# Performance work log

Hardware: AMD Instinct MI355X
Metric: run time of the kernel (lower is better)

The kernel has to match this reference:

```python
import jax, jax.numpy as jnp
import numpy as np

LOG2PI = 1.8378770664093453  # log(2*pi)
TEMP = 0.5  # Gumbel-softmax resampling temperature


def setup_inputs() -> dict:
    key = jax.random.key(0)
    ks = jax.random.split(key, 32)
    B, N, T = 16, 512, 16
    dL, dM, dE, H = 128, 256, 32, 256
    Kt, Ka = 18, 8  # k_regimes + 10 total slots, 8 active
    dIn = dM + dL + dE  # proposal input dim = 416
    r = jax.random.normal

    def w(k, shape):
        return r(k, shape, dtype=jnp.float32) / np.sqrt(shape[0]).astype(np.float32)

    return {
        "obs": r(ks[0], (T, B), dtype=jnp.float32),
        "h_seq": r(ks[1], (T, B, dM), dtype=jnp.float32),
        "z0": r(ks[2], (B, N, dL), dtype=jnp.float32),
        "regime_logits0": r(ks[3], (B, N, Kt), dtype=jnp.float32),
        "eps": r(ks[4], (T, B, N, dL), dtype=jnp.float32),
        "gumbel_u": jax.random.uniform(ks[5], (T, B, N, N), dtype=jnp.float32),
        # LearnedProposal params
        "pe_emb": w(ks[6], (Kt, dE)),
        "pz_w1": w(ks[7], (dIn, H)), "pz_b1": jnp.zeros((H,)),
        "pz_w2": w(ks[8], (H, H)), "pz_b2": jnp.zeros((H,)),
        "pz_w3": w(ks[9], (H, 2 * dL)), "pz_b3": jnp.zeros((2 * dL,)),
        "pr_w1": w(ks[10], (dIn, H)), "pr_b1": jnp.zeros((H,)),
        "pr_w2": w(ks[11], (H, 8)), "pr_b2": jnp.zeros((8,)),
        # ObservationV3 params
        "oe_w1": w(ks[12], (dL + dM, 256)), "oe_b1": jnp.zeros((256,)),
        "oe_w2": w(ks[13], (256, 128)), "oe_b2": jnp.zeros((128,)),
        "oe_w3": w(ks[14], (128, 2)), "oe_b3": jnp.zeros((2,)),
        "log_obs_scale": jnp.zeros((Kt,)),
        "k_active": 8,
    }


def reference(obs, h_seq, z0, regime_logits0, eps, gumbel_u,
              pe_emb, pz_w1, pz_b1, pz_w2, pz_b2, pz_w3, pz_b3,
              pr_w1, pr_b1, pr_w2, pr_b2,
              oe_w1, oe_b1, oe_w2, oe_b2, oe_w3, oe_b3,
              log_obs_scale, k_active):
    B, N, dL = z0.shape
    Kt = regime_logits0.shape[-1]
    silu = jax.nn.silu
    emb_a = pe_emb[:k_active]                               # (Ka, dE)
    scales = jax.nn.softplus(log_obs_scale[:k_active])      # (Ka,)

    def step(carry, xs):
        z, rl, log_w = carry
        h_t, y_t, eps_t, u_t = xs
        h_exp = jnp.broadcast_to(h_t[:, None, :], (B, N, h_t.shape[-1]))
        # --- LearnedProposal ---
        rp = jax.nn.softmax(rl, axis=-1)[:, :, :k_active]
        remb = rp @ emb_a                                   # (B,N,dE)
        inp = jnp.concatenate([h_exp, z, remb], axis=-1)
        hz = silu(inp @ pz_w1 + pz_b1)
        hz = silu(hz @ pz_w2 + pz_b2)
        zp = hz @ pz_w3 + pz_b3
        z_mean = zp[..., :dL]
        z_log_std = jnp.clip(zp[..., dL:], -5.0, 2.0)
        z_new = z_mean + eps_t * jnp.exp(z_log_std)
        log_q = jnp.sum(-0.5 * eps_t**2 - z_log_std - 0.5 * LOG2PI, axis=-1)
        rlog = silu(inp @ pr_w1 + pr_b1) @ pr_w2 + pr_b2    # (B,N,Ka)
        rlog = jnp.concatenate(
            [rlog, jnp.zeros((B, N, Kt - rlog.shape[-1]), rlog.dtype)], axis=-1)
        # --- ObservationV3.log_likelihood ---
        em = silu(jnp.concatenate([z_new, h_exp], axis=-1) @ oe_w1 + oe_b1)
        em = silu(em @ oe_w2 + oe_b2)
        em = em @ oe_w3 + oe_b3
        pred, lsb = em[..., 0], em[..., 1]
        rp_new = jax.nn.softmax(rlog, axis=-1)[:, :, :k_active]
        sigma = jnp.clip(jax.nn.softplus(lsb) * (rp_new @ scales), 0.1, 5.0)
        ll = -0.5 * ((y_t[:, None] - pred) / sigma)**2 - jnp.log(sigma) - 0.5 * LOG2PI
        log_w = log_w + ll - log_q
        # weighted mean output (before resampling resets weights)
        w = jax.nn.softmax(log_w, axis=-1)
        mean_z = jnp.sum(w[..., None] * z_new, axis=1)      # (B,dL)
        # --- soft_resample_v3 (Gumbel-softmax bmm) ---
        g = -jnp.log(-jnp.log(u_t + 1e-10) + 1e-10)
        A = jax.nn.softmax((log_w[:, None, :] + g) / TEMP, axis=-1)  # (B,N,N)
        z_r = jnp.einsum('bij,bjd->bid', A, z_new)
        rl_r = jnp.einsum('bij,bjk->bik', A, rlog)
        return (z_r, rl_r, jnp.zeros_like(log_w)), mean_z

    init = (z0, regime_logits0, jnp.zeros((B, N), z0.dtype))
    _, means = jax.lax.scan(step, init, (h_seq, obs, eps, gumbel_u))
    return means  # (T, B, d_latent)
```

## Files before the change

kernel.cpp:

```cpp
#include <hip/hip_runtime.h>
#include <hip/hip_bf16.h>
#include <math.h>

#define LOG2PI 1.8378770664093453f

constexpr int Bb = 16, Nn = 512, Tt = 16;
constexpr int dL = 128, dM = 256, dE = 32, Kt = 18;
constexpr int P = Bb * Nn;
constexpr int BLK = 32;
constexpr int LDA = 520;
constexpr int LDB = 264;
constexpr int LDE = 136;
constexpr int LDZX = 132;
constexpr int LDR = 40;

typedef __attribute__((ext_vector_type(8))) _Float16 f16x8;
typedef __attribute__((ext_vector_type(4))) float f32x4;

__device__ __forceinline__ float siluf(float x) { return x / (1.f + expf(-x)); }
__device__ __forceinline__ float softplusf(float x) {
    return (x > 20.f) ? x : log1pf(expf(x));
}
__device__ __forceinline__ short f2h(float x) {
    _Float16 h = (_Float16)x;
    short s;
    __builtin_memcpy(&s, &h, 2);
    return s;
}
__device__ __forceinline__ float h2f(short s) {
    _Float16 h;
    __builtin_memcpy(&h, &s, 2);
    return (float)h;
}
__device__ __forceinline__ void split2(float x, short& hi, short& lo) {
    hi = f2h(x);
    lo = f2h(x - h2f(hi));
}
__device__ __forceinline__ f32x4 mfma16(f16x8 a, f16x8 b, f32x4 c) {
    return __builtin_amdgcn_mfma_f32_16x16x32_f16(a, b, c, 0, 0, 0);
}

template<int NF>
__device__ __forceinline__ void mfma_bn(
    const f16x8 (&ah)[2], const f16x8 (&al)[2],
    const short* __restrict__ Whi, const short* __restrict__ Wlo,
    int Kw, int k0, int n0, int lr, int lk, f32x4 (&acc)[2][NF])
{
    #pragma unroll
    for (int nf = 0; nf < NF; nf++) {
        size_t bo = (size_t)(n0 + nf * 16 + lr) * Kw + k0 + lk;
        f16x8 bh = *reinterpret_cast<const f16x8*>(Whi + bo);
        f16x8 bl = *reinterpret_cast<const f16x8*>(Wlo + bo);
        #pragma unroll
        for (int mf = 0; mf < 2; mf++) {
            acc[mf][nf] = mfma16(ah[mf], bh, acc[mf][nf]);
            acc[mf][nf] = mfma16(ah[mf], bl, acc[mf][nf]);
            acc[mf][nf] = mfma16(al[mf], bh, acc[mf][nf]);
        }
    }
}

template<int NF, int KB, int KE, int KW>
__device__ __forceinline__ void gemm_lds(
    const short* lAhi, const short* lAlo, int ldA, int akoff,
    const short* __restrict__ Whi, const short* __restrict__ Wlo,
    int n0, int lr, int lk, f32x4 (&acc)[2][NF])
{
    #pragma unroll 2
    for (int k0 = KB; k0 < KE; k0 += 32) {
        f16x8 ah[2], al[2];
        #pragma unroll
        for (int mf = 0; mf < 2; mf++) {
            int ao = (mf * 16 + lr) * ldA + (k0 - akoff) + lk;
            ah[mf] = *reinterpret_cast<const f16x8*>(lAhi + ao);
            al[mf] = *reinterpret_cast<const f16x8*>(lAlo + ao);
        }
        mfma_bn<NF>(ah, al, Whi, Wlo, KW, k0, n0, lr, lk, acc);
    }
}

template<int NF>
__device__ __forceinline__ void epi_silu(
    f32x4 (&acc)[2][NF], const float* biasw,
    short* outHi, short* outLo, int ldOut, int outBase, int lr, int l4)
{
    #pragma unroll
    for (int nf = 0; nf < NF; nf++) {
        float bv = biasw[nf * 16 + lr];
        #pragma unroll
        for (int mf = 0; mf < 2; mf++) {
            #pragma unroll
            for (int r = 0; r < 4; r++) {
                int row = mf * 16 + l4 + r;
                int col = outBase + nf * 16 + lr;
                float sv = siluf(acc[mf][nf][r] + bv);
                short hi, lo;
                split2(sv, hi, lo);
                outHi[row * ldOut + col] = hi;
                outLo[row * ldOut + col] = lo;
            }
        }
    }
}

struct SMem {
    short actAhi[BLK * LDA], actAlo[BLK * LDA];
    short actBhi[BLK * LDB], actBlo[BLK * LDB];
    short e2hi[BLK * LDE], e2lo[BLK * LDE];
    short hhhi[256], hhlo[256];
    short rembhi[BLK * LDR], remblo[BLK * LDR];
    float zlsx[BLK * LDZX];
    float peL[256];
    float probs[BLK * 8];
    float rlogL[BLK * 8];
    float lqp[4 * BLK];
};

__global__ __launch_bounds__(512) void mega(
    const float* __restrict__ zc, const float* __restrict__ rl,
    const float* __restrict__ h_t, const float* __restrict__ pe_emb,
    const float* __restrict__ eps_t, const float* __restrict__ obs_t,
    const short* __restrict__ w_l1h, const short* __restrict__ w_l1l,
    const short* __restrict__ w_pz2h, const short* __restrict__ w_pz2l,
    const short* __restrict__ w_pz3h, const short* __restrict__ w_pz3l,
    const short* __restrict__ w_oe1h, const short* __restrict__ w_oe1l,
    const short* __restrict__ w_oe2h, const short* __restrict__ w_oe2l,
    const float* __restrict__ pz_b1, const float* __restrict__ pr_b1,
    const float* __restrict__ pz_b2, const float* __restrict__ pz_b3,
    const float* __restrict__ oe_b1, const float* __restrict__ oe_b2,
    const float* __restrict__ pr_w2, const float* __restrict__ pr_b2,
    const float* __restrict__ oe_w3, const float* __restrict__ oe_b3,
    const float* __restrict__ los,
    float* __restrict__ log_w,
    short* __restrict__ vthi, short* __restrict__ vtlo)
{
    __shared__ SMem sm;
    const int tid = threadIdx.x;
    const int wv = tid >> 6, l = tid & 63;
    const int lr = l & 15, lk = (l >> 4) * 8, l4 = (l >> 4) * 4;
    const int p0 = blockIdx.x * BLK;
    const int b = p0 >> 9;
    const int i0 = p0 & 511;

    {
        if (tid < 256) {
            const float* hb = h_t + b * dM;
            short hi, lo;
            split2(hb[tid], hi, lo);
            sm.hhhi[tid] = hi; sm.hhlo[tid] = lo;
            sm.peL[tid] = pe_emb[tid];
        } else {
            int q = tid - 256;
            int pp = q >> 3, cc = q & 7;
            vthi[((size_t)b * 144 + 136 + cc) * 512 + i0 + pp] = 0;
            vtlo[((size_t)b * 144 + 136 + cc) * 512 + i0 + pp] = 0;
        }
        if (tid < BLK) {
            int p = tid;
            float v[Kt], m = -1e30f;
            #pragma unroll
            for (int k = 0; k < Kt; k++) {
                v[k] = rl[(size_t)(p0 + p) * Kt + k];
                m = fmaxf(m, v[k]);
            }
            float denom = 0.f;
            #pragma unroll
            for (int k = 0; k < Kt; k++) denom += expf(v[k] - m);
            #pragma unroll
            for (int k = 0; k < 8; k++)
                sm.probs[p * 8 + k] = expf(v[k] - m) / denom;
        }
    }
    __syncthreads();
    {
        #pragma unroll
        for (int it = 0; it < 2; it++) {
            int idx = it * 512 + tid;
            int p = idx >> 5, d = idx & 31;
            float acc = 0.f;
            #pragma unroll
            for (int kk = 0; kk < 8; kk++)
                acc = fmaf(sm.probs[p * 8 + kk], sm.peL[kk * 32 + d], acc);
            short hi, lo;
            split2(acc, hi, lo);
            sm.rembhi[p * LDR + d] = hi;
            sm.remblo[p * LDR + d] = lo;
        }
    }
    __syncthreads();

    {
        f32x4 acc1[2][4];
        #pragma unroll
        for (int mf = 0; mf < 2; mf++)
            #pragma unroll
            for (int nf = 0; nf < 4; nf++) acc1[mf][nf] = f32x4{0.f, 0.f, 0.f, 0.f};
        int n0 = wv * 64;
        gemm_lds<4, 0, 256, 416>(sm.hhhi, sm.hhlo, 0, 0, w_l1h, w_l1l, n0, lr, lk, acc1);
        #pragma unroll 2
        for (int k0 = 256; k0 < 384; k0 += 32) {
            f16x8 ah[2], al[2];
            #pragma unroll
            for (int mf = 0; mf < 2; mf++) {
                const float* zr = zc + (size_t)(p0 + mf * 16 + lr) * dL + (k0 - 256) + lk;
                #pragma unroll
                for (int j = 0; j < 8; j++) {
                    float zv = zr[j];
                    _Float16 h = (_Float16)zv;
                    ah[mf][j] = h;
                    al[mf][j] = (_Float16)(zv - (float)h);
                }
            }
            mfma_bn<4>(ah, al, w_l1h, w_l1l, 416, k0, n0, lr, lk, acc1);
        }
        gemm_lds<4, 384, 416, 416>(sm.rembhi, sm.remblo, LDR, 384, w_l1h, w_l1l, n0, lr, lk, acc1);
        const float* biasw = (n0 < 256) ? (pz_b1 + n0) : (pr_b1 + (n0 - 256));
        epi_silu<4>(acc1, biasw, sm.actAhi, sm.actAlo, LDA, n0, lr, l4);
    }
    __syncthreads();

    {
        f32x4 acc2[2][2];
        #pragma unroll
        for (int mf = 0; mf < 2; mf++)
            #pragma unroll
            for (int nf = 0; nf < 2; nf++) acc2[mf][nf] = f32x4{0.f, 0.f, 0.f, 0.f};
        int n0 = wv * 32;
        gemm_lds<2, 0, 256, 256>(sm.actAhi, sm.actAlo, LDA, 0, w_pz2h, w_pz2l, n0, lr, lk, acc2);
        epi_silu<2>(acc2, pz_b2 + n0, sm.actBhi, sm.actBlo, LDB, n0, lr, l4);
    }
    __syncthreads();

    {
        f32x4 acc3[2][2];
        #pragma unroll
        for (int mf = 0; mf < 2; mf++)
            #pragma unroll
            for (int nf = 0; nf < 2; nf++) acc3[mf][nf] = f32x4{0.f, 0.f, 0.f, 0.f};
        int n0 = wv * 32;
        gemm_lds<2, 0, 256, 256>(sm.actBhi, sm.actBlo, LDB, 0, w_pz3h, w_pz3l, n0, lr, lk, acc3);
        if (wv >= 4) {
            #pragma unroll
            for (int nf = 0; nf < 2; nf++) {
                int col = n0 + nf * 16 + lr;
                float bv = pz_b3[col];
                #pragma unroll
                for (int mf = 0; mf < 2; mf++)
                    #pragma unroll
                    for (int r = 0; r < 4; r++) {
                        int row = mf * 16 + l4 + r;
                        float zls = fminf(fmaxf(acc3[mf][nf][r] + bv, -5.f), 2.f);
                        sm.zlsx[row * LDZX + (col - 128)] = zls;
                    }
            }
        }
        __syncthreads();
        if (wv < 4) {
            float rowsum[8] = {};
            #pragma unroll
            for (int nf = 0; nf < 2; nf++) {
                int d = n0 + nf * 16 + lr;
                float bv = pz_b3[d];
                #pragma unroll
                for (int mf = 0; mf < 2; mf++)
                    #pragma unroll
                    for (int r = 0; r < 4; r++) {
                        int row = mf * 16 + l4 + r;
                        float zm = acc3[mf][nf][r] + bv;
                        float zls = sm.zlsx[row * LDZX + d];
                        float e = eps_t[(size_t)(p0 + row) * dL + d];
                        float zn = zm + e * expf(zls);
                        short hi, lo;
                        split2(zn, hi, lo);
                        sm.e2hi[row * LDE + d] = hi;
                        sm.e2lo[row * LDE + d] = lo;
                        rowsum[mf * 4 + r] += -0.5f * e * e - zls;
                    }
            }
            #pragma unroll
            for (int o = 1; o < 16; o <<= 1)
                #pragma unroll
                for (int j = 0; j < 8; j++)
                    rowsum[j] += __shfl_xor(rowsum[j], o);
            if (lr == 0) {
                #pragma unroll
                for (int j = 0; j < 8; j++) {
                    int row = (j >> 2) * 16 + l4 + (j & 3);
                    sm.lqp[wv * BLK + row] = rowsum[j];
                }
            }
        }
    }
    __syncthreads();

    #pragma unroll
    for (int it = 0; it < 8; it++) {
        int idx = it * 512 + tid;
        int d = idx >> 5, row = idx & 31;
        vthi[((size_t)b * 144 + d) * 512 + i0 + row] = sm.e2hi[row * LDE + d];
        vtlo[((size_t)b * 144 + d) * 512 + i0 + row] = sm.e2lo[row * LDE + d];
    }

    {
        int p = tid >> 4, s = tid & 15;
        float a8[8] = {};
        for (int kk = s * 16; kk < s * 16 + 16; kk++) {
            float hv = h2f(sm.actAhi[p * LDA + 256 + kk]) +
                       h2f(sm.actAlo[p * LDA + 256 + kk]);
            #pragma unroll
            for (int r = 0; r < 8; r++) a8[r] = fmaf(hv, pr_w2[kk * 8 + r], a8[r]);
        }
        #pragma unroll
        for (int o = 1; o < 16; o <<= 1)
            #pragma unroll
            for (int r = 0; r < 8; r++) a8[r] += __shfl_xor(a8[r], o);
        if (s == 0) {
            #pragma unroll
            for (int r = 0; r < 8; r++) {
                float v = a8[r] + pr_b2[r];
                sm.rlogL[p * 8 + r] = v;
                short hi, lo;
                split2(v, hi, lo);
                vthi[((size_t)b * 144 + 128 + r) * 512 + i0 + p] = hi;
                vtlo[((size_t)b * 144 + 128 + r) * 512 + i0 + p] = lo;
            }
        }
    }
    __syncthreads();

    {
        f32x4 acc5[2][2];
        #pragma unroll
        for (int mf = 0; mf < 2; mf++)
            #pragma unroll
            for (int nf = 0; nf < 2; nf++) acc5[mf][nf] = f32x4{0.f, 0.f, 0.f, 0.f};
        int n0 = wv * 32;
        gemm_lds<2, 0, 256, 384>(sm.hhhi, sm.hhlo, 0, 0, w_oe1h, w_oe1l, n0, lr, lk, acc5);
        gemm_lds<2, 256, 384, 384>(sm.e2hi, sm.e2lo, LDE, 256, w_oe1h, w_oe1l, n0, lr, lk, acc5);
        __syncthreads();
        epi_silu<2>(acc5, oe_b1 + n0, sm.actAhi, sm.actAlo, LDA, n0, lr, l4);
    }
    __syncthreads();

    {
        f32x4 acc6[2][1];
        #pragma unroll
        for (int mf = 0; mf < 2; mf++) acc6[mf][0] = f32x4{0.f, 0.f, 0.f, 0.f};
        int n0 = wv * 16;
        gemm_lds<1, 0, 256, 256>(sm.actAhi, sm.actAlo, LDA, 0, w_oe2h, w_oe2l, n0, lr, lk, acc6);
        __syncthreads();
        epi_silu<1>(acc6, oe_b2 + n0, sm.e2hi, sm.e2lo, LDE, n0, lr, l4);
    }
    __syncthreads();

    {
        int p = tid >> 4, s = tid & 15;
        float q0 = 0.f, q1 = 0.f;
        for (int k = s * 8; k < s * 8 + 8; k++) {
            float e = h2f(sm.e2hi[p * LDE + k]) + h2f(sm.e2lo[p * LDE + k]);
            q0 = fmaf(e, oe_w3[2 * k], q0);
            q1 = fmaf(e, oe_w3[2 * k + 1], q1);
        }
        #pragma unroll
        for (int o = 1; o < 16; o <<= 1) {
            q0 += __shfl_xor(q0, o);
            q1 += __shfl_xor(q1, o);
        }
        if (s == 0) {
            float pred = q0 + oe_b3[0];
            float lsb  = q1 + oe_b3[1];
            float rv[8], m = 0.f;
            #pragma unroll
            for (int r = 0; r < 8; r++) {
                rv[r] = sm.rlogL[p * 8 + r];
                m = fmaxf(m, rv[r]);
            }
            float denom = (Kt - 8) * expf(-m);
            #pragma unroll
            for (int r = 0; r < 8; r++) denom += expf(rv[r] - m);
            float sdot = 0.f;
            #pragma unroll
            for (int r = 0; r < 8; r++)
                sdot += (expf(rv[r] - m) / denom) * softplusf(los[r]);
            float sigma = fminf(fmaxf(softplusf(lsb) * sdot, 0.1f), 5.f);
            float y = obs_t[b];
            float dd = (y - pred) / sigma;
            float ll = -0.5f * dd * dd - logf(sigma) - 0.5f * LOG2PI;
            float lq = sm.lqp[p] + sm.lqp[BLK + p] + sm.lqp[2 * BLK + p]
                     + sm.lqp[3 * BLK + p] - dL * 0.5f * LOG2PI;
            log_w[p0 + p] = ll - lq;
        }
    }
}

__global__ __launch_bounds__(256) void kT(
    const float* __restrict__ in, short* __restrict__ oh, short* __restrict__ ol,
    int K, int N, int ostride, int ooff)
{
    int idx = blockIdx.x * 256 + threadIdx.x;
    if (idx < K * N) {
        int n = idx / K, k = idx % K;
        short hi, lo;
        split2(in[(size_t)k * N + n], hi, lo);
        oh[(size_t)n * ostride + ooff + k] = hi;
        ol[(size_t)n * ostride + ooff + k] = lo;
    }
}

__global__ __launch_bounds__(256) void k11x(
    const float* __restrict__ log_w, const float* __restrict__ u_t,
    short* __restrict__ Ahi, short* __restrict__ Alo,
    short* __restrict__ Ameanhi, short* __restrict__ Ameanlo,
    float* __restrict__ rl)
{
    int wave = threadIdx.x >> 6, lane = threadIdx.x & 63;
    if (blockIdx.x < P / 4) {
        int row = blockIdx.x * 4 + wave;
        int b = row >> 9;
        float q[8], m = -1e30f;
        #pragma unroll
        for (int jj = 0; jj < 8; jj++) {
            int j = jj * 64 + lane;
            float u = u_t[(size_t)row * Nn + j];
            float g = -logf(-logf(u + 1e-10f) + 1e-10f);
            q[jj] = (log_w[b * Nn + j] + g) * 2.0f;
            m = fmaxf(m, q[jj]);
        }
        #pragma unroll
        for (int o = 1; o < 64; o <<= 1) m = fmaxf(m, __shfl_xor(m, o));
        float e[8], s = 0.f;
        #pragma unroll
        for (int jj = 0; jj < 8; jj++) { e[jj] = expf(q[jj] - m); s += e[jj]; }
        #pragma unroll
        for (int o = 1; o < 64; o <<= 1) s += __shfl_xor(s, o);
        float inv = 1.f / s;
        #pragma unroll
        for (int jj = 0; jj < 8; jj++) {
            short hi, lo;
            split2(e[jj] * inv, hi, lo);
            Ahi[(size_t)row * Nn + jj * 64 + lane] = hi;
            Alo[(size_t)row * Nn + jj * 64 + lane] = lo;
        }
        if (lane < 10) rl[row * Kt + 8 + lane] = 0.f;
    } else {
        int b = (blockIdx.x - P / 4) * 4 + wave;
        float q[8], m = -1e30f;
        #pragma unroll
        for (int jj = 0; jj < 8; jj++) {
            q[jj] = log_w[b * Nn + jj * 64 + lane];
            m = fmaxf(m, q[jj]);
        }
        #pragma unroll
        for (int o = 1; o < 64; o <<= 1) m = fmaxf(m, __shfl_xor(m, o));
        float e[8], s = 0.f;
        #pragma unroll
        for (int jj = 0; jj < 8; jj++) { e[jj] = expf(q[jj] - m); s += e[jj]; }
        #pragma unroll
        for (int o = 1; o < 64; o <<= 1) s += __shfl_xor(s, o);
        float inv = 1.f / s;
        #pragma unroll
        for (int jj = 0; jj < 8; jj++) {
            short hi, lo;
            split2(e[jj] * inv, hi, lo);
            Ameanhi[(size_t)b * Nn + jj * 64 + lane] = hi;
            Ameanlo[(size_t)b * Nn + jj * 64 + lane] = lo;
        }
    }
}

__global__ __launch_bounds__(256) void k12x(
    const short* __restrict__ Ahi, const short* __restrict__ Alo,
    const short* __restrict__ Ameanhi, const short* __restrict__ Ameanlo,
    const short* __restrict__ vthi, const short* __restrict__ vtlo,
    float* __restrict__ z, float* __restrict__ rl, float* __restrict__ out_t)
{
    int tid = threadIdx.x;
    int w = tid >> 6, l = tid & 63;
    int lr = l & 15, lk = (l >> 4) * 8;
    int b = blockIdx.x;
    int n0 = blockIdx.z * 48;
    size_t voff = ((size_t)b * 144 + n0 + lr) * 512 + lk;

    if (blockIdx.y == 8) {
        if (w != 0) return;
        f32x4 acc[3];
        #pragma unroll
        for (int nf = 0; nf < 3; nf++) acc[nf] = f32x4{0.f, 0.f, 0.f, 0.f};
        for (int k0 = 0; k0 < 512; k0 += 32) {
            f16x8 ah, al;
            #pragma unroll
            for (int j = 0; j < 8; j++) { ah[j] = (_Float16)0.f; al[j] = (_Float16)0.f; }
            if (lr == 0) {
                ah = *reinterpret_cast<const f16x8*>(Ameanhi + (size_t)b * Nn + k0 + lk);
                al = *reinterpret_cast<const f16x8*>(Ameanlo + (size_t)b * Nn + k0 + lk);
            }
            #pragma unroll
            for (int nf = 0; nf < 3; nf++) {
                size_t bo = voff + (size_t)nf * 16 * 512 + k0;
                f16x8 bh = *reinterpret_cast<const f16x8*>(vthi + bo);
                f16x8 bl = *reinterpret_cast<const f16x8*>(vtlo + bo);
                acc[nf] = mfma16(ah, bh, acc[nf]);
                acc[nf] = mfma16(ah, bl, acc[nf]);
                acc[nf] = mfma16(al, bh, acc[nf]);
            }
        }
        if ((l >> 4) == 0) {
            #pragma unroll
            for (int nf = 0; nf < 3; nf++) {
                int col = n0 + nf * 16 + lr;
                if (col < 128) out_t[b * dL + col] = acc[nf][0];
            }
        }
        return;
    }

    int m0 = blockIdx.y * 64 + w * 16;
    size_t aoff = ((size_t)(b * 512 + m0 + lr)) * 512 + lk;
    f32x4 acc[3];
    #pragma unroll
    for (int nf = 0; nf < 3; nf++) acc[nf] = f32x4{0.f, 0.f, 0.f, 0.f};
    for (int k0 = 0; k0 < 512; k0 += 32) {
        f16x8 ah = *reinterpret_cast<const f16x8*>(Ahi + aoff + k0);
        f16x8 al = *reinterpret_cast<const f16x8*>(Alo + aoff + k0);
        #pragma unroll
        for (int nf = 0; nf < 3; nf++) {
            size_t bo = voff + (size_t)nf * 16 * 512 + k0;
            f16x8 bh = *reinterpret_cast<const f16x8*>(vthi + bo);
            f16x8 bl = *reinterpret_cast<const f16x8*>(vtlo + bo);
            acc[nf] = mfma16(ah, bh, acc[nf]);
            acc[nf] = mfma16(ah, bl, acc[nf]);
            acc[nf] = mfma16(al, bh, acc[nf]);
        }
    }
    int orow = (l >> 4) * 4;
    #pragma unroll
    for (int nf = 0; nf < 3; nf++) {
        int col = n0 + nf * 16 + lr;
        #pragma unroll
        for (int r = 0; r < 4; r++) {
            int gp = b * 512 + m0 + orow + r;
            float v = acc[nf][r];
            if (col < 128) z[(size_t)gp * dL + col] = v;
            else if (col < 136) rl[gp * Kt + (col - 128)] = v;
        }
    }
}

extern "C" void kernel_launch(void* const* d_in, const int* in_sizes, int n_in,
                              void* d_out, int out_size, void* d_ws, size_t ws_size,
                              hipStream_t stream)
{
    const float* obs      = (const float*)d_in[0];
    const float* h_seq    = (const float*)d_in[1];
    const float* z0       = (const float*)d_in[2];
    const float* rl0      = (const float*)d_in[3];
    const float* eps      = (const float*)d_in[4];
    const float* gum      = (const float*)d_in[5];
    const float* pe_emb   = (const float*)d_in[6];
    const float* pz_w1    = (const float*)d_in[7];
    const float* pz_b1    = (const float*)d_in[8];
    const float* pz_w2    = (const float*)d_in[9];
    const float* pz_b2    = (const float*)d_in[10];
    const float* pz_w3    = (const float*)d_in[11];
    const float* pz_b3    = (const float*)d_in[12];
    const float* pr_w1    = (const float*)d_in[13];
    const float* pr_b1    = (const float*)d_in[14];
    const float* pr_w2    = (const float*)d_in[15];
    const float* pr_b2    = (const float*)d_in[16];
    const float* oe_w1    = (const float*)d_in[17];
    const float* oe_b1    = (const float*)d_in[18];
    const float* oe_w2    = (const float*)d_in[19];
    const float* oe_b2    = (const float*)d_in[20];
    const float* oe_w3    = (const float*)d_in[21];
    const float* oe_b3    = (const float*)d_in[22];
    const float* los      = (const float*)d_in[23];
    float* out = (float*)d_out;

    char* base = (char*)d_ws;
    float* z      = (float*)base;  base += (size_t)P * dL * 4;
    float* rl     = (float*)base;  base += (size_t)P * Kt * 4;
    float* log_w  = (float*)base;  base += (size_t)P * 4;
    short* vthi   = (short*)base;  base += (size_t)16 * 144 * 512 * 2;
    short* vtlo   = (short*)base;  base += (size_t)16 * 144 * 512 * 2;
    short* Ahi    = (short*)base;  base += (size_t)P * 512 * 2;
    short* Alo    = (short*)base;  base += (size_t)P * 512 * 2;
    short* Amhi   = (short*)base;  base += (size_t)16 * 512 * 2;
    short* Amlo   = (short*)base;  base += (size_t)16 * 512 * 2;
    short* w_l1h  = (short*)base;  base += (size_t)512 * 416 * 2;
    short* w_l1l  = (short*)base;  base += (size_t)512 * 416 * 2;
    short* w_pz2h = (short*)base;  base += (size_t)256 * 256 * 2;
    short* w_pz2l = (short*)base;  base += (size_t)256 * 256 * 2;
    short* w_pz3h = (short*)base;  base += (size_t)256 * 256 * 2;
    short* w_pz3l = (short*)base;  base += (size_t)256 * 256 * 2;
    short* w_oe1h = (short*)base;  base += (size_t)256 * 384 * 2;
    short* w_oe1l = (short*)base;  base += (size_t)256 * 384 * 2;
    short* w_oe2h = (short*)base;  base += (size_t)128 * 256 * 2;
    short* w_oe2l = (short*)base;  base += (size_t)128 * 256 * 2;

    kT<<<(416 * 256 + 255) / 256, 256, 0, stream>>>(pz_w1, w_l1h, w_l1l, 416, 256, 416, 0);
    kT<<<(416 * 256 + 255) / 256, 256, 0, stream>>>(
        pr_w1, w_l1h + (size_t)256 * 416, w_l1l + (size_t)256 * 416, 416, 256, 416, 0);
    kT<<<(256 * 256 + 255) / 256, 256, 0, stream>>>(pz_w2, w_pz2h, w_pz2l, 256, 256, 256, 0);
    kT<<<(256 * 256 + 255) / 256, 256, 0, stream>>>(pz_w3, w_pz3h, w_pz3l, 256, 256, 256, 0);
    kT<<<(256 * 256 + 255) / 256, 256, 0, stream>>>(
        oe_w1 + (size_t)128 * 256, w_oe1h, w_oe1l, 256, 256, 384, 0);
    kT<<<(128 * 256 + 255) / 256, 256, 0, stream>>>(
        oe_w1, w_oe1h, w_oe1l, 128, 256, 384, 256);
    kT<<<(256 * 128 + 255) / 256, 256, 0, stream>>>(oe_w2, w_oe2h, w_oe2l, 256, 128, 256, 0);

    (void)hipMemcpyAsync(z, z0, (size_t)P * dL * sizeof(float),
                         hipMemcpyDeviceToDevice, stream);
    (void)hipMemcpyAsync(rl, rl0, (size_t)P * Kt * sizeof(float),
                         hipMemcpyDeviceToDevice, stream);

    for (int t = 0; t < Tt; t++) {
        const float* h_t   = h_seq + (size_t)t * Bb * dM;
        const float* obs_t = obs + (size_t)t * Bb;
        const float* eps_t = eps + (size_t)t * P * dL;
        const float* u_t   = gum + (size_t)t * P * Nn;
        float* out_t = out + (size_t)t * Bb * dL;

        mega<<<P / BLK, 512, 0, stream>>>(
            z, rl, h_t, pe_emb, eps_t, obs_t,
            w_l1h, w_l1l, w_pz2h, w_pz2l, w_pz3h, w_pz3l,
            w_oe1h, w_oe1l, w_oe2h, w_oe2l,
            pz_b1, pr_b1, pz_b2, pz_b3, oe_b1, oe_b2,
            pr_w2, pr_b2, oe_w3, oe_b3, los,
            log_w, vthi, vtlo);
        k11x<<<P / 4 + 4, 256, 0, stream>>>(log_w, u_t, Ahi, Alo,
                                            Amhi, Amlo, rl);
        k12x<<<dim3(16, 9, 3), 256, 0, stream>>>(Ahi, Alo, Amhi, Amlo,
                                                 vthi, vtlo, z, rl, out_t);
    }
}
```

Baseline: 2.050 ms.

## Halve particle block size to 16 rows per workgroup in fused step kernel

Cuts the per-workgroup particle tile from 32 to 16 rows. The MFMA helpers, epilogues and reductions are reworked for a single 16-row fragment, and the thread-to-row mappings in the small reductions are adjusted. This doubles the number of workgroups (512 instead of 256) so the MI355X's many CUs get more work, but every weight fragment loaded from global or L2 now feeds half as many MFMAs, lowering weight reuse and arithmetic intensity.

```diff
diff --git a/kernel.cpp b/kernel.cpp
--- a/kernel.cpp
+++ b/kernel.cpp
@@ -7,7 +7,7 @@
 constexpr int Bb = 16, Nn = 512, Tt = 16;
 constexpr int dL = 128, dM = 256, dE = 32, Kt = 18;
 constexpr int P = Bb * Nn;
-constexpr int BLK = 32;
+constexpr int BLK = 16;
 constexpr int LDA = 520;
 constexpr int LDB = 264;
 constexpr int LDE = 136;
@@ -41,64 +41,54 @@
 }
 
 template<int NF>
-__device__ __forceinline__ void mfma_bn(
-    const f16x8 (&ah)[2], const f16x8 (&al)[2],
+__device__ __forceinline__ void mfma_bn1(
+    f16x8 ah, f16x8 al,
     const short* __restrict__ Whi, const short* __restrict__ Wlo,
-    int Kw, int k0, int n0, int lr, int lk, f32x4 (&acc)[2][NF])
+    int Kw, int k0, int n0, int lr, int lk, f32x4 (&acc)[NF])
 {
     #pragma unroll
     for (int nf = 0; nf < NF; nf++) {
         size_t bo = (size_t)(n0 + nf * 16 + lr) * Kw + k0 + lk;
         f16x8 bh = *reinterpret_cast<const f16x8*>(Whi + bo);
         f16x8 bl = *reinterpret_cast<const f16x8*>(Wlo + bo);
-        #pragma unroll
-        for (int mf = 0; mf < 2; mf++) {
-            acc[mf][nf] = mfma16(ah[mf], bh, acc[mf][nf]);
-            acc[mf][nf] = mfma16(ah[mf], bl, acc[mf][nf]);
-            acc[mf][nf] = mfma16(al[mf], bh, acc[mf][nf]);
-        }
+        acc[nf] = mfma16(ah, bh, acc[nf]);
+        acc[nf] = mfma16(ah, bl, acc[nf]);
+        acc[nf] = mfma16(al, bh, acc[nf]);
     }
 }
 
 template<int NF, int KB, int KE, int KW>
-__device__ __forceinline__ void gemm_lds(
+__device__ __forceinline__ void gemm_lds1(
     const short* lAhi, const short* lAlo, int ldA, int akoff,
     const short* __restrict__ Whi, const short* __restrict__ Wlo,
-    int n0, int lr, int lk, f32x4 (&acc)[2][NF])
+    int n0, int lr, int lk, f32x4 (&acc)[NF])
 {
     #pragma unroll 2
     for (int k0 = KB; k0 < KE; k0 += 32) {
-        f16x8 ah[2], al[2];
-        #pragma unroll
-        for (int mf = 0; mf < 2; mf++) {
-            int ao = (mf * 16 + lr) * ldA + (k0 - akoff) + lk;
-            ah[mf] = *reinterpret_cast<const f16x8*>(lAhi + ao);
-            al[mf] = *reinterpret_cast<const f16x8*>(lAlo + ao);
-        }
-        mfma_bn<NF>(ah, al, Whi, Wlo, KW, k0, n0, lr, lk, acc);
+        int ao = lr * ldA + (k0 - akoff) + lk;
+        f16x8 ah = *reinterpret_cast<const f16x8*>(lAhi + ao);
+        f16x8 al = *reinterpret_cast<const f16x8*>(lAlo + ao);
+        mfma_bn1<NF>(ah, al, Whi, Wlo, KW, k0, n0, lr, lk, acc);
     }
 }
 
 template<int NF>
-__device__ __forceinline__ void epi_silu(
-    f32x4 (&acc)[2][NF], const float* biasw,
+__device__ __forceinline__ void epi_silu1(
+    f32x4 (&acc)[NF], const float* biasw,
     short* outHi, short* outLo, int ldOut, int outBase, int lr, int l4)
 {
     #pragma unroll
     for (int nf = 0; nf < NF; nf++) {
         float bv = biasw[nf * 16 + lr];
         #pragma unroll
-        for (int mf = 0; mf < 2; mf++) {
-            #pragma unroll
-            for (int r = 0; r < 4; r++) {
-                int row = mf * 16 + l4 + r;
-                int col = outBase + nf * 16 + lr;
-                float sv = siluf(acc[mf][nf][r] + bv);
-                short hi, lo;
-                split2(sv, hi, lo);
-                outHi[row * ldOut + col] = hi;
-                outLo[row * ldOut + col] = lo;
-            }
+        for (int r = 0; r < 4; r++) {
+            int row = l4 + r;
+            int col = outBase + nf * 16 + lr;
+            float sv = siluf(acc[nf][r] + bv);
+            short hi, lo;
+            split2(sv, hi, lo);
+            outHi[row * ldOut + col] = hi;
+            outLo[row * ldOut + col] = lo;
         }
     }
 }
@@ -149,7 +139,7 @@
             split2(hb[tid], hi, lo);
             sm.hhhi[tid] = hi; sm.hhlo[tid] = lo;
             sm.peL[tid] = pe_emb[tid];
-        } else {
+        } else if (tid < 384) {
             int q = tid - 256;
             int pp = q >> 3, cc = q & 7;
             vthi[((size_t)b * 144 + 136 + cc) * 512 + i0 + pp] = 0;
@@ -173,145 +163,126 @@
     }
     __syncthreads();
     {
-        #pragma unroll
-        for (int it = 0; it < 2; it++) {
-            int idx = it * 512 + tid;
-            int p = idx >> 5, d = idx & 31;
-            float acc = 0.f;
-            #pragma unroll
-            for (int kk = 0; kk < 8; kk++)
-                acc = fmaf(sm.probs[p * 8 + kk], sm.peL[kk * 32 + d], acc);
-            short hi, lo;
-            split2(acc, hi, lo);
-            sm.rembhi[p * LDR + d] = hi;
-            sm.remblo[p * LDR + d] = lo;
-        }
-    }
-    __syncthreads();
-
-    {
-        f32x4 acc1[2][4];
-        #pragma unroll
-        for (int mf = 0; mf < 2; mf++)
-            #pragma unroll
-            for (int nf = 0; nf < 4; nf++) acc1[mf][nf] = f32x4{0.f, 0.f, 0.f, 0.f};
+        int p = tid >> 5, d = tid & 31;
+        float acc = 0.f;
+        #pragma unroll
+        for (int kk = 0; kk < 8; kk++)
+            acc = fmaf(sm.probs[p * 8 + kk], sm.peL[kk * 32 + d], acc);
+        short hi, lo;
+        split2(acc, hi, lo);
+        sm.rembhi[p * LDR + d] = hi;
+        sm.remblo[p * LDR + d] = lo;
+    }
+    __syncthreads();
+
+    {
+        f32x4 acc1[4];
+        #pragma unroll
+        for (int nf = 0; nf < 4; nf++) acc1[nf] = f32x4{0.f, 0.f, 0.f, 0.f};
         int n0 = wv * 64;
-        gemm_lds<4, 0, 256, 416>(sm.hhhi, sm.hhlo, 0, 0, w_l1h, w_l1l, n0, lr, lk, acc1);
+        gemm_lds1<4, 0, 256, 416>(sm.hhhi, sm.hhlo, 0, 0, w_l1h, w_l1l, n0, lr, lk, acc1);
         #pragma unroll 2
         for (int k0 = 256; k0 < 384; k0 += 32) {
-            f16x8 ah[2], al[2];
-            #pragma unroll
-            for (int mf = 0; mf < 2; mf++) {
-                const float* zr = zc + (size_t)(p0 + mf * 16 + lr) * dL + (k0 - 256) + lk;
-                #pragma unroll
-                for (int j = 0; j < 8; j++) {
-                    float zv = zr[j];
-                    _Float16 h = (_Float16)zv;
-                    ah[mf][j] = h;
-                    al[mf][j] = (_Float16)(zv - (float)h);
-                }
-            }
-            mfma_bn<4>(ah, al, w_l1h, w_l1l, 416, k0, n0, lr, lk, acc1);
-        }
-        gemm_lds<4, 384, 416, 416>(sm.rembhi, sm.remblo, LDR, 384, w_l1h, w_l1l, n0, lr, lk, acc1);
+            f16x8 ah, al;
+            const float* zr = zc + (size_t)(p0 + lr) * dL + (k0 - 256) + lk;
+            #pragma unroll
+            for (int j = 0; j < 8; j++) {
+                float zv = zr[j];
+                _Float16 h = (_Float16)zv;
+                ah[j] = h;
+                al[j] = (_Float16)(zv - (float)h);
+            }
+            mfma_bn1<4>(ah, al, w_l1h, w_l1l, 416, k0, n0, lr, lk, acc1);
+        }
+        gemm_lds1<4, 384, 416, 416>(sm.rembhi, sm.remblo, LDR, 384, w_l1h, w_l1l, n0, lr, lk, acc1);
         const float* biasw = (n0 < 256) ? (pz_b1 + n0) : (pr_b1 + (n0 - 256));
-        epi_silu<4>(acc1, biasw, sm.actAhi, sm.actAlo, LDA, n0, lr, l4);
-    }
-    __syncthreads();
-
-    {
-        f32x4 acc2[2][2];
-        #pragma unroll
-        for (int mf = 0; mf < 2; mf++)
-            #pragma unroll
-            for (int nf = 0; nf < 2; nf++) acc2[mf][nf] = f32x4{0.f, 0.f, 0.f, 0.f};
+        epi_silu1<4>(acc1, biasw, sm.actAhi, sm.actAlo, LDA, n0, lr, l4);
+    }
+    __syncthreads();
+
+    {
+        f32x4 acc2[2];
+        acc2[0] = f32x4{0.f, 0.f, 0.f, 0.f};
+        acc2[1] = f32x4{0.f, 0.f, 0.f, 0.f};
         int n0 = wv * 32;
-        gemm_lds<2, 0, 256, 256>(sm.actAhi, sm.actAlo, LDA, 0, w_pz2h, w_pz2l, n0, lr, lk, acc2);
-        epi_silu<2>(acc2, pz_b2 + n0, sm.actBhi, sm.actBlo, LDB, n0, lr, l4);
-    }
-    __syncthreads();
-
-    {
-        f32x4 acc3[2][2];
-        #pragma unroll
-        for (int mf = 0; mf < 2; mf++)
-            #pragma unroll
-            for (int nf = 0; nf < 2; nf++) acc3[mf][nf] = f32x4{0.f, 0.f, 0.f, 0.f};
+        gemm_lds1<2, 0, 256, 256>(sm.actAhi, sm.actAlo, LDA, 0, w_pz2h, w_pz2l, n0, lr, lk, acc2);
+        epi_silu1<2>(acc2, pz_b2 + n0, sm.actBhi, sm.actBlo, LDB, n0, lr, l4);
+    }
+    __syncthreads();
+
+    {
+        f32x4 acc3[2];
+        acc3[0] = f32x4{0.f, 0.f, 0.f, 0.f};
+        acc3[1] = f32x4{0.f, 0.f, 0.f, 0.f};
         int n0 = wv * 32;
-        gemm_lds<2, 0, 256, 256>(sm.actBhi, sm.actBlo, LDB, 0, w_pz3h, w_pz3l, n0, lr, lk, acc3);
+        gemm_lds1<2, 0, 256, 256>(sm.actBhi, sm.actBlo, LDB, 0, w_pz3h, w_pz3l, n0, lr, lk, acc3);
         if (wv >= 4) {
             #pragma unroll
             for (int nf = 0; nf < 2; nf++) {
                 int col = n0 + nf * 16 + lr;
                 float bv = pz_b3[col];
                 #pragma unroll
-                for (int mf = 0; mf < 2; mf++)
-                    #pragma unroll
-                    for (int r = 0; r < 4; r++) {
-                        int row = mf * 16 + l4 + r;
-                        float zls = fminf(fmaxf(acc3[mf][nf][r] + bv, -5.f), 2.f);
-                        sm.zlsx[row * LDZX + (col - 128)] = zls;
-                    }
+                for (int r = 0; r < 4; r++) {
+                    int row = l4 + r;
+                    float zls = fminf(fmaxf(acc3[nf][r] + bv, -5.f), 2.f);
+                    sm.zlsx[row * LDZX + (col - 128)] = zls;
+                }
             }
         }
         __syncthreads();
         if (wv < 4) {
-            float rowsum[8] = {};
+            float rowsum[4] = {};
             #pragma unroll
             for (int nf = 0; nf < 2; nf++) {
                 int d = n0 + nf * 16 + lr;
                 float bv = pz_b3[d];
                 #pragma unroll
-                for (int mf = 0; mf < 2; mf++)
-                    #pragma unroll
-                    for (int r = 0; r < 4; r++) {
-                        int row = mf * 16 + l4 + r;
-                        float zm = acc3[mf][nf][r] + bv;
-                        float zls = sm.zlsx[row * LDZX + d];
-                        float e = eps_t[(size_t)(p0 + row) * dL + d];
-                        float zn = zm + e * expf(zls);
-                        short hi, lo;
-                        split2(zn, hi, lo);
-                        sm.e2hi[row * LDE + d] = hi;
-                        sm.e2lo[row * LDE + d] = lo;
-                        rowsum[mf * 4 + r] += -0.5f * e * e - zls;
-                    }
+                for (int r = 0; r < 4; r++) {
+                    int row = l4 + r;
+                    float zm = acc3[nf][r] + bv;
+                    float zls = sm.zlsx[row * LDZX + d];
+                    float e = eps_t[(size_t)(p0 + row) * dL + d];
+                    float zn = zm + e * expf(zls);
+                    short hi, lo;
+                    split2(zn, hi, lo);
+                    sm.e2hi[row * LDE + d] = hi;
+                    sm.e2lo[row * LDE + d] = lo;
+                    rowsum[r] += -0.5f * e * e - zls;
+                }
             }
             #pragma unroll
             for (int o = 1; o < 16; o <<= 1)
                 #pragma unroll
-                for (int j = 0; j < 8; j++)
+                for (int j = 0; j < 4; j++)
                     rowsum[j] += __shfl_xor(rowsum[j], o);
             if (lr == 0) {
                 #pragma unroll
-                for (int j = 0; j < 8; j++) {
-                    int row = (j >> 2) * 16 + l4 + (j & 3);
-                    sm.lqp[wv * BLK + row] = rowsum[j];
-                }
+                for (int j = 0; j < 4; j++)
+                    sm.lqp[wv * BLK + l4 + j] = rowsum[j];
             }
         }
     }
     __syncthreads();
 
     #pragma unroll
-    for (int it = 0; it < 8; it++) {
+    for (int it = 0; it < 4; it++) {
         int idx = it * 512 + tid;
-        int d = idx >> 5, row = idx & 31;
+        int d = idx >> 4, row = idx & 15;
         vthi[((size_t)b * 144 + d) * 512 + i0 + row] = sm.e2hi[row * LDE + d];
         vtlo[((size_t)b * 144 + d) * 512 + i0 + row] = sm.e2lo[row * LDE + d];
     }
 
     {
-        int p = tid >> 4, s = tid & 15;
+        int p = tid >> 5, s = tid & 31;
         float a8[8] = {};
-        for (int kk = s * 16; kk < s * 16 + 16; kk++) {
+        for (int kk = s * 8; kk < s * 8 + 8; kk++) {
             float hv = h2f(sm.actAhi[p * LDA + 256 + kk]) +
                        h2f(sm.actAlo[p * LDA + 256 + kk]);
             #pragma unroll
             for (int r = 0; r < 8; r++) a8[r] = fmaf(hv, pr_w2[kk * 8 + r], a8[r]);
         }
         #pragma unroll
-        for (int o = 1; o < 16; o <<= 1)
+        for (int o = 1; o < 32; o <<= 1)
             #pragma unroll
             for (int r = 0; r < 8; r++) a8[r] += __shfl_xor(a8[r], o);
         if (s == 0) {
@@ -329,40 +300,37 @@
     __syncthreads();
 
     {
-        f32x4 acc5[2][2];
-        #pragma unroll
-        for (int mf = 0; mf < 2; mf++)
-            #pragma unroll
-            for (int nf = 0; nf < 2; nf++) acc5[mf][nf] = f32x4{0.f, 0.f, 0.f, 0.f};
+        f32x4 acc5[2];
+        acc5[0] = f32x4{0.f, 0.f, 0.f, 0.f};
+        acc5[1] = f32x4{0.f, 0.f, 0.f, 0.f};
         int n0 = wv * 32;
-        gemm_lds<2, 0, 256, 384>(sm.hhhi, sm.hhlo, 0, 0, w_oe1h, w_oe1l, n0, lr, lk, acc5);
-        gemm_lds<2, 256, 384, 384>(sm.e2hi, sm.e2lo, LDE, 256, w_oe1h, w_oe1l, n0, lr, lk, acc5);
+        gemm_lds1<2, 0, 256, 384>(sm.hhhi, sm.hhlo, 0, 0, w_oe1h, w_oe1l, n0, lr, lk, acc5);
+        gemm_lds1<2, 256, 384, 384>(sm.e2hi, sm.e2lo, LDE, 256, w_oe1h, w_oe1l, n0, lr, lk, acc5);
         __syncthreads();
-        epi_silu<2>(acc5, oe_b1 + n0, sm.actAhi, sm.actAlo, LDA, n0, lr, l4);
-    }
-    __syncthreads();
-
-    {
-        f32x4 acc6[2][1];
-        #pragma unroll
-        for (int mf = 0; mf < 2; mf++) acc6[mf][0] = f32x4{0.f, 0.f, 0.f, 0.f};
+        epi_silu1<2>(acc5, oe_b1 + n0, sm.actAhi, sm.actAlo, LDA, n0, lr, l4);
+    }
+    __syncthreads();
+
+    {
+        f32x4 acc6[1];
+        acc6[0] = f32x4{0.f, 0.f, 0.f, 0.f};
         int n0 = wv * 16;
-        gemm_lds<1, 0, 256, 256>(sm.actAhi, sm.actAlo, LDA, 0, w_oe2h, w_oe2l, n0, lr, lk, acc6);
+        gemm_lds1<1, 0, 256, 256>(sm.actAhi, sm.actAlo, LDA, 0, w_oe2h, w_oe2l, n0, lr, lk, acc6);
         __syncthreads();
-        epi_silu<1>(acc6, oe_b2 + n0, sm.e2hi, sm.e2lo, LDE, n0, lr, l4);
-    }
-    __syncthreads();
-
-    {
-        int p = tid >> 4, s = tid & 15;
+        epi_silu1<1>(acc6, oe_b2 + n0, sm.e2hi, sm.e2lo, LDE, n0, lr, l4);
+    }
+    __syncthreads();
+
+    {
+        int p = tid >> 5, s = tid & 31;
         float q0 = 0.f, q1 = 0.f;
-        for (int k = s * 8; k < s * 8 + 8; k++) {
+        for (int k = s * 4; k < s * 4 + 4; k++) {
             float e = h2f(sm.e2hi[p * LDE + k]) + h2f(sm.e2lo[p * LDE + k]);
             q0 = fmaf(e, oe_w3[2 * k], q0);
             q1 = fmaf(e, oe_w3[2 * k + 1], q1);
         }
         #pragma unroll
-        for (int o = 1; o < 16; o <<= 1) {
+        for (int o = 1; o < 32; o <<= 1) {
             q0 += __shfl_xor(q0, o);
             q1 += __shfl_xor(q1, o);
         }
```

New measurement: 2.529 ms. 1.23x slower.
